# Kernel tuning notes

Measured on AMD Instinct MI355X. Metric: run time of the kernel, lower is better.

Reference implementation:

```python
import jax, jax.numpy as jnp
import numpy as np

N_CLASSES = 8  # hardcoded by the (-1, 8, 8) reshape in the original layer

def setup_inputs() -> dict:
    key = jax.random.key(0)
    k1, k2, k3, k4 = jax.random.split(key, 4)
    B, F, C, R = 16384, 128, N_CLASSES, 64
    x = jax.random.normal(k1, (B, F), dtype=jnp.float32)
    p = jax.random.uniform(k2, (B, C), dtype=jnp.float32)  # class-prob-like input
    W = jax.random.normal(k3, (F, C * C, R), dtype=jnp.float32) * 0.02
    b = jax.random.normal(k4, (C, C, R), dtype=jnp.float32) * 0.1
    return {"x": x, "p": p, "W": W, "b": b}

def reference(x, p, W, b):
    # x: (B, 128) features; p: (B, C) class probs; W: (128, C*C, R); b: (C, C, R)
    B = x.shape[0]
    C = b.shape[0]
    R = b.shape[-1]
    # per-annotator GEMM fused across all annotators: (B, C*C, R)
    logits = jnp.einsum('bf,fkr->bkr', x, W).reshape(B, C, C, R) + b[None]
    # row-softmax: softmax over the "predicted class" axis for each true class c
    M = jax.nn.softmax(logits, axis=2)  # (B, C, C, R)
    # batched dot: p (B,C) contracted against rows of each annotator matrix
    out = jnp.einsum('bc,bcdr->bdr', p, M)  # (B, C, R)
    # NOTE: original applies K.dropout(0.5) (training-mode); omitted for a
    # deterministic inference reference (identity at eval).
    return out
```

## Files before the change

### kernel.cpp

```cpp
#include <hip/hip_runtime.h>
#include <hip/hip_bf16.h>


#define F_DIM    128
#define NCOL     4096
#define OUT_STRIDE 512
#define LOG2E    1.44269504088896340736f

typedef __bf16 bf16x8 __attribute__((ext_vector_type(8)));
typedef float  f32x4  __attribute__((ext_vector_type(4)));

#define AS1(p) ((const __attribute__((address_space(1))) unsigned int*)(p))
#define AS3(p) ((__attribute__((address_space(3))) unsigned int*)(p))

__global__ void wconv_kernel(const float* __restrict__ W,
                             const float* __restrict__ bias,
                             __bf16* __restrict__ wf,
                             float* __restrict__ biasT) {
    int f    = blockIdx.x * 256 + threadIdx.x;
    int lane = f & 63;
    int tkk  = f >> 6;
    int t    = tkk >> 2;
    int kk   = tkk & 3;
    int kbase = kk * 32 + (lane >> 4) * 8;
    int n     = t * 16 + (lane & 15);
    bf16x8 frag;
#pragma unroll
    for (int j = 0; j < 8; ++j)
        frag[j] = (__bf16)(W[(kbase + j) * NCOL + n] * LOG2E);
    *(bf16x8*)(wf + (size_t)f * 8) = frag;

    if (f < 4096) {
        int c = f >> 9, r = (f >> 3) & 63, d = f & 7;
        biasT[f] = bias[(c * 8 + d) * 64 + r] * LOG2E;
    }
}

__global__ __launch_bounds__(512, 4)
void fused_kernel(const float* __restrict__ x, const float* __restrict__ p,
                  const float* __restrict__ biasT, const __bf16* __restrict__ wf,
                  float* __restrict__ out) {
    __shared__ __align__(16) char lds[65536];

    const int lane = threadIdx.x & 63;
    const int ww   = threadIdx.x >> 6;
    const int quad = lane >> 4;
    const int l15  = lane & 15;
    const int w    = blockIdx.x >> 7;
    const int g    = blockIdx.x & 127;
    const int b0   = g * 128 + ww * 16;

    {
        const __bf16* src = wf + (size_t)((ww * 4 + w) * 4) * 512 + lane * 8;
#pragma unroll
        for (int kk = 0; kk < 4; ++kk)
            __builtin_amdgcn_global_load_lds(
                AS1(src + kk * 512),
                AS3(lds + (ww * 4 + kk) * 1024), 16, 0, 0);
    }

    bf16x8 afr[4];
    {
        const float* xr = x + (size_t)(b0 + l15) * F_DIM + quad * 8;
#pragma unroll
        for (int kk = 0; kk < 4; ++kk) {
            float4 lo = *(const float4*)(xr + kk * 32);
            float4 hi = *(const float4*)(xr + kk * 32 + 4);
            bf16x8 f;
            f[0] = (__bf16)lo.x; f[1] = (__bf16)lo.y;
            f[2] = (__bf16)lo.z; f[3] = (__bf16)lo.w;
            f[4] = (__bf16)hi.x; f[5] = (__bf16)hi.y;
            f[6] = (__bf16)hi.z; f[7] = (__bf16)hi.w;
            afr[kk] = f;
        }
    }

    float O[8][4] = {};

#pragma unroll 1
    for (int c = 0; c < 8; ++c) {
        __syncthreads();

        float pvv[4];
#pragma unroll
        for (int jj = 0; jj < 4; ++jj)
            pvv[jj] = p[(size_t)(b0 + quad * 4 + jj) * 8 + c];

        f32x4 bv0 = *(const f32x4*)(biasT + (c * 64 + w * 16 + l15) * 8);
        f32x4 bv1 = *(const f32x4*)(biasT + (c * 64 + w * 16 + l15) * 8 + 4);

        if (c < 7) {
            const __bf16* src =
                wf + (size_t)((((c + 1) * 8 + ww) * 4 + w) * 4) * 512 + lane * 8;
            char* dst = lds + ((c + 1) & 1) * 32768;
#pragma unroll
            for (int kk = 0; kk < 4; ++kk)
                __builtin_amdgcn_global_load_lds(
                    AS1(src + kk * 512),
                    AS3(dst + (ww * 4 + kk) * 1024), 16, 0, 0);
        }

        const char* buf = lds + (c & 1) * 32768;
        f32x4 acc[8];
#pragma unroll
        for (int d = 0; d < 8; ++d) {
            float bvd = (d < 4) ? bv0[d & 3] : bv1[d & 3];
            f32x4 a = {bvd, bvd, bvd, bvd};
#pragma unroll
            for (int kk = 0; kk < 4; ++kk) {
                bf16x8 bfr = *(const bf16x8*)(buf + (d * 4 + kk) * 1024 + lane * 16);
                a = __builtin_amdgcn_mfma_f32_16x16x32_bf16(afr[kk], bfr, a, 0, 0, 0);
            }
#pragma unroll
            for (int jj = 0; jj < 4; ++jj)
                a[jj] = __builtin_amdgcn_exp2f(a[jj]);
            acc[d] = a;
        }

#pragma unroll
        for (int jj = 0; jj < 4; ++jj) {
            float s01 = acc[0][jj] + acc[1][jj], s23 = acc[2][jj] + acc[3][jj];
            float s45 = acc[4][jj] + acc[5][jj], s67 = acc[6][jj] + acc[7][jj];
            float s = (s01 + s23) + (s45 + s67);
            float scale = pvv[jj] * __builtin_amdgcn_rcpf(s);
#pragma unroll
            for (int d = 0; d < 8; ++d)
                O[d][jj] = __builtin_fmaf(acc[d][jj], scale, O[d][jj]);
        }
    }

#pragma unroll
    for (int jj = 0; jj < 4; ++jj) {
        float* orow = out + (size_t)(b0 + quad * 4 + jj) * OUT_STRIDE + w * 16 + l15;
#pragma unroll
        for (int d = 0; d < 8; ++d)
            __builtin_nontemporal_store(O[d][jj], orow + d * 64);
    }
}

extern "C" void kernel_launch(void* const* d_in, const int* in_sizes, int n_in,
                              void* d_out, int out_size, void* d_ws, size_t ws_size,
                              hipStream_t stream) {
    const float* x    = (const float*)d_in[0];
    const float* p    = (const float*)d_in[1];
    const float* W    = (const float*)d_in[2];
    const float* bias = (const float*)d_in[3];
    float* out = (float*)d_out;
    __bf16* wf    = (__bf16*)d_ws;
    float*  biasT = (float*)((char*)d_ws + (1 << 20));

    wconv_kernel<<<dim3(256), dim3(256), 0, stream>>>(W, bias, wf, biasT);
    fused_kernel<<<dim3(512), dim3(512), 0, stream>>>(x, p, biasT, wf, out);
}
```

Baseline: 98.46 us.

## Use 1024-thread blocks with 4-deep LDS ring processing two classes per barrier

```diff
diff --git a/kernel.cpp b/kernel.cpp
--- a/kernel.cpp
+++ b/kernel.cpp
@@ -36,27 +36,31 @@
     }
 }
 
-__global__ __launch_bounds__(512, 4)
+__global__ __launch_bounds__(1024, 4)
 void fused_kernel(const float* __restrict__ x, const float* __restrict__ p,
                   const float* __restrict__ biasT, const __bf16* __restrict__ wf,
                   float* __restrict__ out) {
-    __shared__ __align__(16) char lds[65536];
+    __shared__ __align__(16) char lds[131072];
 
     const int lane = threadIdx.x & 63;
     const int ww   = threadIdx.x >> 6;
     const int quad = lane >> 4;
     const int l15  = lane & 15;
-    const int w    = blockIdx.x >> 7;
-    const int g    = blockIdx.x & 127;
-    const int b0   = g * 128 + ww * 16;
+    const int w    = blockIdx.x >> 6;
+    const int g    = blockIdx.x & 63;
+    const int b0   = g * 256 + ww * 16;
 
-    {
-        const __bf16* src = wf + (size_t)((ww * 4 + w) * 4) * 512 + lane * 8;
+    const int fi0 = ww * 2;
+    const int d0s = fi0 >> 2;
+    const int kk0 = fi0 & 3;
+
 #pragma unroll
-        for (int kk = 0; kk < 4; ++kk)
-            __builtin_amdgcn_global_load_lds(
-                AS1(src + kk * 512),
-                AS3(lds + (ww * 4 + kk) * 1024), 16, 0, 0);
+    for (int c = 0; c < 2; ++c) {
+        char* dst = lds + c * 32768;
+        const __bf16* src =
+            wf + (size_t)(((c * 8 + d0s) * 4 + w) * 4 + kk0) * 512 + lane * 8;
+        __builtin_amdgcn_global_load_lds(AS1(src),       AS3(dst + fi0 * 1024),       16, 0, 0);
+        __builtin_amdgcn_global_load_lds(AS1(src + 512), AS3(dst + fi0 * 1024 + 1024), 16, 0, 0);
     }
 
     bf16x8 afr[4];
@@ -77,10 +81,7 @@
 
     float O[8][4] = {};
 
-#pragma unroll 1
-    for (int c = 0; c < 8; ++c) {
-        __syncthreads();
-
+    auto compute_c = [&](int c, const char* buf) {
         float pvv[4];
 #pragma unroll
         for (int jj = 0; jj < 4; ++jj)
@@ -89,18 +90,6 @@
         f32x4 bv0 = *(const f32x4*)(biasT + (c * 64 + w * 16 + l15) * 8);
         f32x4 bv1 = *(const f32x4*)(biasT + (c * 64 + w * 16 + l15) * 8 + 4);
 
-        if (c < 7) {
-            const __bf16* src =
-                wf + (size_t)((((c + 1) * 8 + ww) * 4 + w) * 4) * 512 + lane * 8;
-            char* dst = lds + ((c + 1) & 1) * 32768;
-#pragma unroll
-            for (int kk = 0; kk < 4; ++kk)
-                __builtin_amdgcn_global_load_lds(
-                    AS1(src + kk * 512),
-                    AS3(dst + (ww * 4 + kk) * 1024), 16, 0, 0);
-        }
-
-        const char* buf = lds + (c & 1) * 32768;
         f32x4 acc[8];
 #pragma unroll
         for (int d = 0; d < 8; ++d) {
@@ -127,6 +116,27 @@
             for (int d = 0; d < 8; ++d)
                 O[d][jj] = __builtin_fmaf(acc[d][jj], scale, O[d][jj]);
         }
+    };
+
+#pragma unroll 1
+    for (int wi = 0; wi < 4; ++wi) {
+        const int c0 = wi * 2;
+        __syncthreads();
+
+        if (wi < 3) {
+#pragma unroll
+            for (int u = 2; u < 4; ++u) {
+                int c = c0 + u;
+                char* dst = lds + (c & 3) * 32768;
+                const __bf16* src =
+                    wf + (size_t)(((c * 8 + d0s) * 4 + w) * 4 + kk0) * 512 + lane * 8;
+                __builtin_amdgcn_global_load_lds(AS1(src),       AS3(dst + fi0 * 1024),        16, 0, 0);
+                __builtin_amdgcn_global_load_lds(AS1(src + 512), AS3(dst + fi0 * 1024 + 1024), 16, 0, 0);
+            }
+        }
+
+        compute_c(c0,     lds + (c0 & 3) * 32768);
+        compute_c(c0 + 1, lds + ((c0 + 1) & 3) * 32768);
     }
 
 #pragma unroll
@@ -150,5 +160,5 @@
     float*  biasT = (float*)((char*)d_ws + (1 << 20));
 
     wconv_kernel<<<dim3(256), dim3(256), 0, stream>>>(W, bias, wf, biasT);
-    fused_kernel<<<dim3(512), dim3(512), 0, stream>>>(x, p, biasT, wf, out);
+    fused_kernel<<<dim3(256), dim3(1024), 0, stream>>>(x, p, biasT, wf, out);
 }
```

Result: slower. 104.3 us (+6.0%).
